# Kernel optimization log

Hardware: AMD Instinct MI355X
Metric: run time of the kernel (lower is better)

## Reference

```python
import jax, jax.numpy as jnp
import numpy as np

NUM_STEPS = 100
ALPHA = 0.9      # learn_alpha=False default in snn.Synaptic
THRESHOLD = 1.0
SLOPE = 25.0     # fast_sigmoid default slope

@jax.custom_vjp
def spike_fn(x):
    # Heaviside forward with fast-sigmoid surrogate gradient
    return (x > 0).astype(x.dtype)

def _spike_fwd(x):
    return (x > 0).astype(x.dtype), x

def _spike_bwd(x, g):
    return (g / (SLOPE * jnp.abs(x) + 1.0) ** 2,)

spike_fn.defvjp(_spike_fwd, _spike_bwd)


def setup_inputs() -> dict:
    key = jax.random.key(0)
    k0, k1, k2 = jax.random.split(key, 3)
    B, NI, NH, NO = 4096, 256, 2048, 128
    x = jax.random.normal(k0, (B, NI), dtype=jnp.float32)
    # Linear init scale ~ 1/sqrt(fan_in)
    W1 = jax.random.normal(k1, (NH, NI), dtype=jnp.float32) / np.sqrt(NI)
    b1 = jnp.zeros((NH,), dtype=jnp.float32)
    W2 = jax.random.normal(k2, (NO, NH), dtype=jnp.float32) / np.sqrt(NH)
    b2 = jnp.zeros((NO,), dtype=jnp.float32)
    beta = jnp.asarray(0.85, dtype=jnp.float32)  # learnable scalar
    return {"x": x, "W1": W1, "b1": b1, "W2": W2, "b2": b2, "beta": beta}


def reference(x, W1, b1, W2, b2, beta):
    # cur1 = fc1(x) is identical every step -> hoist (same math)
    cur1 = x @ W1.T + b1                      # [B, NH]
    beta_c = jnp.clip(beta, 0.0, 1.0)
    B, NH = cur1.shape
    z = jnp.zeros((B, NH), dtype=cur1.dtype)

    def step(carry, _):
        syn, mem, _spk = carry
        # reset-by-subtraction from detached pre-update membrane
        reset = jax.lax.stop_gradient((mem > THRESHOLD).astype(mem.dtype))
        syn = ALPHA * syn + cur1
        mem = beta_c * mem + syn - reset * THRESHOLD
        spk = spike_fn(mem - THRESHOLD)
        return (syn, mem, spk), None

    (syn, mem, spk), _ = jax.lax.scan(step, (z, z, z), None, length=NUM_STEPS)
    cur2 = spk @ W2.T + b2                    # [B, NO]
    return cur2
```

## Files before the change

kernel.cpp:

```cpp
#include <hip/hip_runtime.h>
#include <stdint.h>


typedef __attribute__((ext_vector_type(8))) short short8;
typedef __attribute__((ext_vector_type(4))) float floatx4;

#define NSTEPS 100

static __device__ __forceinline__ uint32_t f2bf2(float lo, float hi) {
  union { float f; uint32_t u; } a, b; a.f = lo; b.f = hi;
  uint32_t x = (a.u + 0x7FFFu + ((a.u >> 16) & 1u)) >> 16;
  uint32_t y = (b.u + 0x7FFFu + ((b.u >> 16) & 1u)) & 0xFFFF0000u;
  return x | y;
}

__global__ __launch_bounds__(256, 4) void snn_k1(
    const float* __restrict__ X, const float* __restrict__ W1,
    const float* __restrict__ b1, const float* __restrict__ betap,
    uint16_t* __restrict__ spk)
{
  __shared__ __align__(16) float As[32 * 68];
  __shared__ __align__(16) float Bs[32 * 68];
  const int tid = threadIdx.x;
  const int bm  = blockIdx.y * 64;
  const int bn  = blockIdx.x * 64;
  const int ty  = tid >> 4;
  const int tx  = tid & 15;
  const int sc  = tid & 7;
  const int sr  = tid >> 3;

  float acc[4][4] = {};

  float4 xa[2], wa[2];
  #pragma unroll
  for (int h = 0; h < 2; ++h) {
    const int r = sr + h * 32;
    xa[h] = *(const float4*)(X  + (size_t)(bm + r) * 256 + sc * 4);
    wa[h] = *(const float4*)(W1 + (size_t)(bn + r) * 256 + sc * 4);
  }

  #pragma unroll 1
  for (int k0 = 0; k0 < 256; k0 += 32) {
    #pragma unroll
    for (int h = 0; h < 2; ++h) {
      const int r = sr + h * 32;
      As[(sc * 4 + 0) * 68 + r] = xa[h].x;
      As[(sc * 4 + 1) * 68 + r] = xa[h].y;
      As[(sc * 4 + 2) * 68 + r] = xa[h].z;
      As[(sc * 4 + 3) * 68 + r] = xa[h].w;
      Bs[(sc * 4 + 0) * 68 + r] = wa[h].x;
      Bs[(sc * 4 + 1) * 68 + r] = wa[h].y;
      Bs[(sc * 4 + 2) * 68 + r] = wa[h].z;
      Bs[(sc * 4 + 3) * 68 + r] = wa[h].w;
    }
    __syncthreads();

    if (k0 < 224) {
      const int kn = k0 + 32;
      #pragma unroll
      for (int h = 0; h < 2; ++h) {
        const int r = sr + h * 32;
        xa[h] = *(const float4*)(X  + (size_t)(bm + r) * 256 + kn + sc * 4);
        wa[h] = *(const float4*)(W1 + (size_t)(bn + r) * 256 + kn + sc * 4);
      }
    }

    #pragma unroll
    for (int kk = 0; kk < 32; ++kk) {
      const float4 a4 = *(const float4*)(As + kk * 68 + ty * 4);
      const float4 b4 = *(const float4*)(Bs + kk * 68 + tx * 4);
      const float av[4] = {a4.x, a4.y, a4.z, a4.w};
      const float bv[4] = {b4.x, b4.y, b4.z, b4.w};
      #pragma unroll
      for (int i = 0; i < 4; ++i)
        #pragma unroll
        for (int j = 0; j < 4; ++j)
          acc[i][j] += av[i] * bv[j];
    }
    __syncthreads();
  }

  float beta = betap[0];
  beta = fminf(fmaxf(beta, 0.0f), 1.0f);
  float bias[4];
  #pragma unroll
  for (int j = 0; j < 4; ++j) bias[j] = b1[bn + tx * 4 + j];

  float cc[16];
  #pragma unroll
  for (int i = 0; i < 4; ++i)
    #pragma unroll
    for (int j = 0; j < 4; ++j)
      cc[i * 4 + j] = acc[i][j] + bias[j];

  #pragma unroll
  for (int h = 0; h < 2; ++h) {
    float syn[8], mem[8];
    #pragma unroll
    for (int e = 0; e < 8; ++e) { syn[e] = 0.0f; mem[e] = 0.0f; }

    #pragma unroll 1
    for (int t = 0; t < NSTEPS; ++t) {
      #pragma unroll
      for (int e = 0; e < 8; ++e) {
        const float rst = (mem[e] > 1.0f) ? 1.0f : 0.0f;
        syn[e] = __fadd_rn(__fmul_rn(0.9f, syn[e]), cc[h * 8 + e]);
        mem[e] = __fsub_rn(__fadd_rn(__fmul_rn(beta, mem[e]), syn[e]), rst);
      }
    }

    #pragma unroll
    for (int i = 0; i < 2; ++i) {
      ushort4 o;
      o.x = (mem[i * 4 + 0] > 1.0f) ? (uint16_t)0x3F80u : (uint16_t)0u;
      o.y = (mem[i * 4 + 1] > 1.0f) ? (uint16_t)0x3F80u : (uint16_t)0u;
      o.z = (mem[i * 4 + 2] > 1.0f) ? (uint16_t)0x3F80u : (uint16_t)0u;
      o.w = (mem[i * 4 + 3] > 1.0f) ? (uint16_t)0x3F80u : (uint16_t)0u;
      *(ushort4*)(spk + (size_t)(bm + ty * 4 + h * 2 + i) * 2048 + bn + tx * 4) = o;
    }
  }
}

#define PS 72

__global__ __launch_bounds__(256) void snn_k2(
    const uint16_t* __restrict__ spk, const float* __restrict__ W2,
    float* __restrict__ part)
{
  __shared__ short As[128 * PS];
  __shared__ short Bs[128 * PS];
  const int tid  = threadIdx.x;
  const int lane = tid & 63;
  const int w    = tid >> 6;
  const int wm   = (w >> 1) * 64;
  const int wn   = (w & 1) * 64;
  const int bm   = blockIdx.x * 128;
  const int kc   = blockIdx.y;

  floatx4 acc[4][4] = {};

  #pragma unroll 1
  for (int kk = 0; kk < 4; ++kk) {
    const int k0 = kc * 256 + kk * 64;
    #pragma unroll
    for (int p = 0; p < 4; ++p) {
      const int u = p * 256 + tid;
      const int r = u >> 3, c = u & 7;
      const int4 va = *(const int4*)(spk + (size_t)(bm + r) * 2048 + k0 + c * 8);
      *(int4*)(As + r * PS + c * 8) = va;
    }
    #pragma unroll
    for (int p = 0; p < 4; ++p) {
      const int u = p * 256 + tid;
      const int n = u >> 3, c = u & 7;
      const float* wp = W2 + (size_t)n * 2048 + k0 + c * 8;
      const float4 w0 = *(const float4*)(wp);
      const float4 w1 = *(const float4*)(wp + 4);
      int4 pk;
      pk.x = (int)f2bf2(w0.x, w0.y);
      pk.y = (int)f2bf2(w0.z, w0.w);
      pk.z = (int)f2bf2(w1.x, w1.y);
      pk.w = (int)f2bf2(w1.z, w1.w);
      *(int4*)(Bs + n * PS + c * 8) = pk;
    }
    __syncthreads();

    #pragma unroll
    for (int ks = 0; ks < 2; ++ks) {
      const int kb = ks * 4 + (lane >> 4);
      const int fe = lane & 15;
      short8 a8[4], b8[4];
      #pragma unroll
      for (int tm = 0; tm < 4; ++tm)
        a8[tm] = *(const short8*)(As + (wm + tm * 16 + fe) * PS + kb * 8);
      #pragma unroll
      for (int tn = 0; tn < 4; ++tn)
        b8[tn] = *(const short8*)(Bs + (wn + tn * 16 + fe) * PS + kb * 8);
      #pragma unroll
      for (int tm = 0; tm < 4; ++tm)
        #pragma unroll
        for (int tn = 0; tn < 4; ++tn)
          acc[tm][tn] = __builtin_amdgcn_mfma_f32_16x16x32_bf16(
              a8[tm], b8[tn], acc[tm][tn], 0, 0, 0);
    }
    __syncthreads();
  }

  const int fe = lane & 15;
  const int fr = (lane >> 4) * 4;
  #pragma unroll
  for (int tm = 0; tm < 4; ++tm)
    #pragma unroll
    for (int tn = 0; tn < 4; ++tn)
      #pragma unroll
      for (int r = 0; r < 4; ++r) {
        const int row = bm + wm + tm * 16 + fr + r;
        const int col = wn + tn * 16 + fe;
        part[((size_t)kc * 4096 + row) * 128 + col] = acc[tm][tn][r];
      }
}

__global__ __launch_bounds__(256) void snn_k3(
    const float* __restrict__ part, const float* __restrict__ b2,
    float* __restrict__ out)
{
  const int idx = blockIdx.x * 256 + threadIdx.x;
  const int m = idx >> 5;
  const int c = (idx & 31) << 2;
  float s0 = 0.f, s1 = 0.f, s2 = 0.f, s3 = 0.f;
  #pragma unroll
  for (int kc = 0; kc < 8; ++kc) {
    const float4 p = *(const float4*)(part + ((size_t)kc * 4096 + m) * 128 + c);
    s0 += p.x; s1 += p.y; s2 += p.z; s3 += p.w;
  }
  float4 o;
  o.x = s0 + b2[c + 0];
  o.y = s1 + b2[c + 1];
  o.z = s2 + b2[c + 2];
  o.w = s3 + b2[c + 3];
  *(float4*)(out + (size_t)m * 128 + c) = o;
}

extern "C" void kernel_launch(void* const* d_in, const int* in_sizes, int n_in,
                              void* d_out, int out_size, void* d_ws, size_t ws_size,
                              hipStream_t stream) {
  const float* X    = (const float*)d_in[0];
  const float* W1   = (const float*)d_in[1];
  const float* b1   = (const float*)d_in[2];
  const float* W2   = (const float*)d_in[3];
  const float* b2   = (const float*)d_in[4];
  const float* beta = (const float*)d_in[5];
  float* out = (float*)d_out;

  uint16_t* spk = (uint16_t*)d_ws;
  float* part = (float*)((char*)d_ws + (size_t)4096 * 2048 * 2);

  snn_k1<<<dim3(32, 64), 256, 0, stream>>>(X, W1, b1, beta, spk);
  snn_k2<<<dim3(32, 8), 256, 0, stream>>>(spk, W2, part);
  snn_k3<<<512, 256, 0, stream>>>(part, b2, out);
}
```

Baseline: 212.1 us.

## Double k1 K-tile and restructure k2 into LDS-free register-fed MFMA with more blocks

The first kernel now stages a 64-wide K slice per iteration instead of 32, which halves the number of barrier and prefetch rounds at the cost of twice the shared memory. The second kernel drops its shared-memory staging entirely. Each wave loads its spike and W2 fragments straight from global memory into MFMA operands over smaller 32x128 output tiles, and the grid grows from 32 to 128 blocks along M. This trades operand reuse through LDS for more parallelism and no barriers, so W2 is re-read and converted to bf16 by more blocks.

```diff
diff --git a/kernel.cpp b/kernel.cpp
--- a/kernel.cpp
+++ b/kernel.cpp
@@ -19,8 +19,8 @@
     const float* __restrict__ b1, const float* __restrict__ betap,
     uint16_t* __restrict__ spk)
 {
-  __shared__ __align__(16) float As[32 * 68];
-  __shared__ __align__(16) float Bs[32 * 68];
+  __shared__ __align__(16) float As[64 * 68];
+  __shared__ __align__(16) float Bs[64 * 68];
   const int tid = threadIdx.x;
   const int bm  = blockIdx.y * 64;
   const int bn  = blockIdx.x * 64;
@@ -31,42 +31,52 @@
 
   float acc[4][4] = {};
 
-  float4 xa[2], wa[2];
+  float4 xa[2][2], wa[2][2];
   #pragma unroll
   for (int h = 0; h < 2; ++h) {
     const int r = sr + h * 32;
-    xa[h] = *(const float4*)(X  + (size_t)(bm + r) * 256 + sc * 4);
-    wa[h] = *(const float4*)(W1 + (size_t)(bn + r) * 256 + sc * 4);
+    #pragma unroll
+    for (int kh = 0; kh < 2; ++kh) {
+      xa[h][kh] = *(const float4*)(X  + (size_t)(bm + r) * 256 + kh * 32 + sc * 4);
+      wa[h][kh] = *(const float4*)(W1 + (size_t)(bn + r) * 256 + kh * 32 + sc * 4);
+    }
   }
 
   #pragma unroll 1
-  for (int k0 = 0; k0 < 256; k0 += 32) {
+  for (int k0 = 0; k0 < 256; k0 += 64) {
     #pragma unroll
     for (int h = 0; h < 2; ++h) {
       const int r = sr + h * 32;
-      As[(sc * 4 + 0) * 68 + r] = xa[h].x;
-      As[(sc * 4 + 1) * 68 + r] = xa[h].y;
-      As[(sc * 4 + 2) * 68 + r] = xa[h].z;
-      As[(sc * 4 + 3) * 68 + r] = xa[h].w;
-      Bs[(sc * 4 + 0) * 68 + r] = wa[h].x;
-      Bs[(sc * 4 + 1) * 68 + r] = wa[h].y;
-      Bs[(sc * 4 + 2) * 68 + r] = wa[h].z;
-      Bs[(sc * 4 + 3) * 68 + r] = wa[h].w;
+      #pragma unroll
+      for (int kh = 0; kh < 2; ++kh) {
+        const int kb = kh * 32 + sc * 4;
+        As[(kb + 0) * 68 + r] = xa[h][kh].x;
+        As[(kb + 1) * 68 + r] = xa[h][kh].y;
+        As[(kb + 2) * 68 + r] = xa[h][kh].z;
+        As[(kb + 3) * 68 + r] = xa[h][kh].w;
+        Bs[(kb + 0) * 68 + r] = wa[h][kh].x;
+        Bs[(kb + 1) * 68 + r] = wa[h][kh].y;
+        Bs[(kb + 2) * 68 + r] = wa[h][kh].z;
+        Bs[(kb + 3) * 68 + r] = wa[h][kh].w;
+      }
     }
     __syncthreads();
 
-    if (k0 < 224) {
-      const int kn = k0 + 32;
+    if (k0 < 192) {
+      const int kn = k0 + 64;
       #pragma unroll
       for (int h = 0; h < 2; ++h) {
         const int r = sr + h * 32;
-        xa[h] = *(const float4*)(X  + (size_t)(bm + r) * 256 + kn + sc * 4);
-        wa[h] = *(const float4*)(W1 + (size_t)(bn + r) * 256 + kn + sc * 4);
-      }
-    }
-
-    #pragma unroll
-    for (int kk = 0; kk < 32; ++kk) {
+        #pragma unroll
+        for (int kh = 0; kh < 2; ++kh) {
+          xa[h][kh] = *(const float4*)(X  + (size_t)(bm + r) * 256 + kn + kh * 32 + sc * 4);
+          wa[h][kh] = *(const float4*)(W1 + (size_t)(bn + r) * 256 + kn + kh * 32 + sc * 4);
+        }
+      }
+    }
+
+    #pragma unroll
+    for (int kk = 0; kk < 64; ++kk) {
       const float4 a4 = *(const float4*)(As + kk * 68 + ty * 4);
       const float4 b4 = *(const float4*)(Bs + kk * 68 + tx * 4);
       const float av[4] = {a4.x, a4.y, a4.z, a4.w};
@@ -121,80 +131,59 @@
   }
 }
 
-#define PS 72
-
 __global__ __launch_bounds__(256) void snn_k2(
     const uint16_t* __restrict__ spk, const float* __restrict__ W2,
     float* __restrict__ part)
 {
-  __shared__ short As[128 * PS];
-  __shared__ short Bs[128 * PS];
   const int tid  = threadIdx.x;
   const int lane = tid & 63;
   const int w    = tid >> 6;
-  const int wm   = (w >> 1) * 64;
-  const int wn   = (w & 1) * 64;
-  const int bm   = blockIdx.x * 128;
+  const int wn   = w * 32;
+  const int bm   = blockIdx.x * 32;
   const int kc   = blockIdx.y;
-
-  floatx4 acc[4][4] = {};
-
-  #pragma unroll 1
-  for (int kk = 0; kk < 4; ++kk) {
-    const int k0 = kc * 256 + kk * 64;
-    #pragma unroll
-    for (int p = 0; p < 4; ++p) {
-      const int u = p * 256 + tid;
-      const int r = u >> 3, c = u & 7;
-      const int4 va = *(const int4*)(spk + (size_t)(bm + r) * 2048 + k0 + c * 8);
-      *(int4*)(As + r * PS + c * 8) = va;
-    }
-    #pragma unroll
-    for (int p = 0; p < 4; ++p) {
-      const int u = p * 256 + tid;
-      const int n = u >> 3, c = u & 7;
-      const float* wp = W2 + (size_t)n * 2048 + k0 + c * 8;
+  const int fe   = lane & 15;
+  const int kq   = lane >> 4;
+
+  floatx4 acc[2][2] = {};
+
+  const uint16_t* a0 = spk + (size_t)(bm + fe) * 2048 + kc * 256 + kq * 8;
+  const uint16_t* a1 = a0 + (size_t)16 * 2048;
+  const float* b0 = W2 + (size_t)(wn + fe) * 2048 + kc * 256 + kq * 8;
+  const float* b1p = b0 + (size_t)16 * 2048;
+
+  #pragma unroll
+  for (int kb = 0; kb < 8; ++kb) {
+    const int ko = kb * 32;
+    short8 a8[2], b8[2];
+    a8[0] = *(const short8*)(a0 + ko);
+    a8[1] = *(const short8*)(a1 + ko);
+    #pragma unroll
+    for (int tn = 0; tn < 2; ++tn) {
+      const float* wp = (tn == 0) ? (b0 + ko) : (b1p + ko);
       const float4 w0 = *(const float4*)(wp);
       const float4 w1 = *(const float4*)(wp + 4);
-      int4 pk;
-      pk.x = (int)f2bf2(w0.x, w0.y);
-      pk.y = (int)f2bf2(w0.z, w0.w);
-      pk.z = (int)f2bf2(w1.x, w1.y);
-      pk.w = (int)f2bf2(w1.z, w1.w);
-      *(int4*)(Bs + n * PS + c * 8) = pk;
-    }
-    __syncthreads();
-
-    #pragma unroll
-    for (int ks = 0; ks < 2; ++ks) {
-      const int kb = ks * 4 + (lane >> 4);
-      const int fe = lane & 15;
-      short8 a8[4], b8[4];
-      #pragma unroll
-      for (int tm = 0; tm < 4; ++tm)
-        a8[tm] = *(const short8*)(As + (wm + tm * 16 + fe) * PS + kb * 8);
-      #pragma unroll
-      for (int tn = 0; tn < 4; ++tn)
-        b8[tn] = *(const short8*)(Bs + (wn + tn * 16 + fe) * PS + kb * 8);
-      #pragma unroll
-      for (int tm = 0; tm < 4; ++tm)
-        #pragma unroll
-        for (int tn = 0; tn < 4; ++tn)
-          acc[tm][tn] = __builtin_amdgcn_mfma_f32_16x16x32_bf16(
-              a8[tm], b8[tn], acc[tm][tn], 0, 0, 0);
-    }
-    __syncthreads();
-  }
-
-  const int fe = lane & 15;
-  const int fr = (lane >> 4) * 4;
-  #pragma unroll
-  for (int tm = 0; tm < 4; ++tm)
-    #pragma unroll
-    for (int tn = 0; tn < 4; ++tn)
+      union { int4 i4; short8 s8; } pk;
+      pk.i4.x = (int)f2bf2(w0.x, w0.y);
+      pk.i4.y = (int)f2bf2(w0.z, w0.w);
+      pk.i4.z = (int)f2bf2(w1.x, w1.y);
+      pk.i4.w = (int)f2bf2(w1.z, w1.w);
+      b8[tn] = pk.s8;
+    }
+    #pragma unroll
+    for (int tm = 0; tm < 2; ++tm)
+      #pragma unroll
+      for (int tn = 0; tn < 2; ++tn)
+        acc[tm][tn] = __builtin_amdgcn_mfma_f32_16x16x32_bf16(
+            a8[tm], b8[tn], acc[tm][tn], 0, 0, 0);
+  }
+
+  #pragma unroll
+  for (int tm = 0; tm < 2; ++tm)
+    #pragma unroll
+    for (int tn = 0; tn < 2; ++tn)
       #pragma unroll
       for (int r = 0; r < 4; ++r) {
-        const int row = bm + wm + tm * 16 + fr + r;
+        const int row = bm + tm * 16 + kq * 4 + r;
         const int col = wn + tn * 16 + fe;
         part[((size_t)kc * 4096 + row) * 128 + col] = acc[tm][tn][r];
       }
@@ -236,6 +225,6 @@
   float* part = (float*)((char*)d_ws + (size_t)4096 * 2048 * 2);
 
   snn_k1<<<dim3(32, 64), 256, 0, stream>>>(X, W1, b1, beta, spk);
-  snn_k2<<<dim3(32, 8), 256, 0, stream>>>(spk, W2, part);
+  snn_k2<<<dim3(128, 8), 256, 0, stream>>>(spk, W2, part);
   snn_k3<<<512, 256, 0, stream>>>(part, b2, out);
 }
```

After: 265.5 us. +25.1%, slower.

## Split GEMM1 and recurrence into separate kernels with larger GEMM tiles

Applied to the files above, without the earlier changes.

The fused GEMM+LIF kernel is split into a 128x128-tile fp32 GEMM that writes cur1 to workspace and a separate elementwise kernel that runs the 100-step recurrence and writes bf16 spikes. The hidden dimension is processed in two halves of 1024 so the cur1 buffer fits in the reused partial-sum workspace. Larger tiles raise arithmetic intensity of GEMM1 and the recurrence kernel gets full occupancy. The cost is an extra round trip of cur1 through global memory and four launches instead of one.

```diff
diff --git a/kernel.cpp b/kernel.cpp
--- a/kernel.cpp
+++ b/kernel.cpp
@@ -14,111 +14,135 @@
   return x | y;
 }
 
-__global__ __launch_bounds__(256, 4) void snn_k1(
-    const float* __restrict__ X, const float* __restrict__ W1,
-    const float* __restrict__ b1, const float* __restrict__ betap,
-    uint16_t* __restrict__ spk)
-{
-  __shared__ __align__(16) float As[32 * 68];
-  __shared__ __align__(16) float Bs[32 * 68];
+__global__ __launch_bounds__(256) void snn_gemm1(
+    const float* __restrict__ X, const float* __restrict__ W1h,
+    const float* __restrict__ b1h, float* __restrict__ cur1h)
+{
+  __shared__ __align__(16) float As[32 * 132];
+  __shared__ __align__(16) float Bs[32 * 132];
   const int tid = threadIdx.x;
-  const int bm  = blockIdx.y * 64;
-  const int bn  = blockIdx.x * 64;
+  const int bn  = blockIdx.x * 128;
+  const int bm  = blockIdx.y * 128;
   const int ty  = tid >> 4;
   const int tx  = tid & 15;
+  const int sr  = tid >> 3;
   const int sc  = tid & 7;
-  const int sr  = tid >> 3;
-
-  float acc[4][4] = {};
-
-  float4 xa[2], wa[2];
-  #pragma unroll
-  for (int h = 0; h < 2; ++h) {
-    const int r = sr + h * 32;
-    xa[h] = *(const float4*)(X  + (size_t)(bm + r) * 256 + sc * 4);
-    wa[h] = *(const float4*)(W1 + (size_t)(bn + r) * 256 + sc * 4);
+
+  float acc[8][8] = {};
+
+  float4 xa[4], wa[4];
+  #pragma unroll
+  for (int h = 0; h < 4; ++h) {
+    const int r = h * 32 + sr;
+    xa[h] = *(const float4*)(X   + (size_t)(bm + r) * 256 + sc * 4);
+    wa[h] = *(const float4*)(W1h + (size_t)(bn + r) * 256 + sc * 4);
   }
 
   #pragma unroll 1
   for (int k0 = 0; k0 < 256; k0 += 32) {
     #pragma unroll
-    for (int h = 0; h < 2; ++h) {
-      const int r = sr + h * 32;
-      As[(sc * 4 + 0) * 68 + r] = xa[h].x;
-      As[(sc * 4 + 1) * 68 + r] = xa[h].y;
-      As[(sc * 4 + 2) * 68 + r] = xa[h].z;
-      As[(sc * 4 + 3) * 68 + r] = xa[h].w;
-      Bs[(sc * 4 + 0) * 68 + r] = wa[h].x;
-      Bs[(sc * 4 + 1) * 68 + r] = wa[h].y;
-      Bs[(sc * 4 + 2) * 68 + r] = wa[h].z;
-      Bs[(sc * 4 + 3) * 68 + r] = wa[h].w;
+    for (int h = 0; h < 4; ++h) {
+      const int r = h * 32 + sr;
+      As[(sc * 4 + 0) * 132 + r] = xa[h].x;
+      As[(sc * 4 + 1) * 132 + r] = xa[h].y;
+      As[(sc * 4 + 2) * 132 + r] = xa[h].z;
+      As[(sc * 4 + 3) * 132 + r] = xa[h].w;
+      Bs[(sc * 4 + 0) * 132 + r] = wa[h].x;
+      Bs[(sc * 4 + 1) * 132 + r] = wa[h].y;
+      Bs[(sc * 4 + 2) * 132 + r] = wa[h].z;
+      Bs[(sc * 4 + 3) * 132 + r] = wa[h].w;
     }
     __syncthreads();
 
     if (k0 < 224) {
       const int kn = k0 + 32;
       #pragma unroll
-      for (int h = 0; h < 2; ++h) {
-        const int r = sr + h * 32;
-        xa[h] = *(const float4*)(X  + (size_t)(bm + r) * 256 + kn + sc * 4);
-        wa[h] = *(const float4*)(W1 + (size_t)(bn + r) * 256 + kn + sc * 4);
+      for (int h = 0; h < 4; ++h) {
+        const int r = h * 32 + sr;
+        xa[h] = *(const float4*)(X   + (size_t)(bm + r) * 256 + kn + sc * 4);
+        wa[h] = *(const float4*)(W1h + (size_t)(bn + r) * 256 + kn + sc * 4);
       }
     }
 
     #pragma unroll
     for (int kk = 0; kk < 32; ++kk) {
-      const float4 a4 = *(const float4*)(As + kk * 68 + ty * 4);
-      const float4 b4 = *(const float4*)(Bs + kk * 68 + tx * 4);
-      const float av[4] = {a4.x, a4.y, a4.z, a4.w};
-      const float bv[4] = {b4.x, b4.y, b4.z, b4.w};
-      #pragma unroll
-      for (int i = 0; i < 4; ++i)
+      const float4 a0 = *(const float4*)(As + kk * 132 + ty * 8);
+      const float4 a1 = *(const float4*)(As + kk * 132 + ty * 8 + 4);
+      const float4 b0 = *(const float4*)(Bs + kk * 132 + tx * 8);
+      const float4 b1 = *(const float4*)(Bs + kk * 132 + tx * 8 + 4);
+      const float av[8] = {a0.x, a0.y, a0.z, a0.w, a1.x, a1.y, a1.z, a1.w};
+      const float bv[8] = {b0.x, b0.y, b0.z, b0.w, b1.x, b1.y, b1.z, b1.w};
+      #pragma unroll
+      for (int i = 0; i < 8; ++i)
         #pragma unroll
-        for (int j = 0; j < 4; ++j)
+        for (int j = 0; j < 8; ++j)
           acc[i][j] += av[i] * bv[j];
     }
     __syncthreads();
   }
+
+  float bias[8];
+  #pragma unroll
+  for (int j = 0; j < 8; ++j) bias[j] = b1h[bn + tx * 8 + j];
+
+  #pragma unroll
+  for (int i = 0; i < 8; ++i) {
+    const int row = bm + ty * 8 + i;
+    float4 o0, o1;
+    o0.x = acc[i][0] + bias[0];
+    o0.y = acc[i][1] + bias[1];
+    o0.z = acc[i][2] + bias[2];
+    o0.w = acc[i][3] + bias[3];
+    o1.x = acc[i][4] + bias[4];
+    o1.y = acc[i][5] + bias[5];
+    o1.z = acc[i][6] + bias[6];
+    o1.w = acc[i][7] + bias[7];
+    *(float4*)(cur1h + (size_t)row * 1024 + bn + tx * 8)     = o0;
+    *(float4*)(cur1h + (size_t)row * 1024 + bn + tx * 8 + 4) = o1;
+  }
+}
+
+__global__ __launch_bounds__(256) void snn_rec(
+    const float* __restrict__ cur1h, const float* __restrict__ betap,
+    uint16_t* __restrict__ spk, int nh0)
+{
+  const int idx = blockIdx.x * 256 + threadIdx.x;
+  const int row = idx >> 7;
+  const int col = (idx & 127) * 8;
+
+  const float4 c0 = *(const float4*)(cur1h + (size_t)row * 1024 + col);
+  const float4 c1 = *(const float4*)(cur1h + (size_t)row * 1024 + col + 4);
+  const float cc[8] = {c0.x, c0.y, c0.z, c0.w, c1.x, c1.y, c1.z, c1.w};
 
   float beta = betap[0];
   beta = fminf(fmaxf(beta, 0.0f), 1.0f);
-  float bias[4];
-  #pragma unroll
-  for (int j = 0; j < 4; ++j) bias[j] = b1[bn + tx * 4 + j];
-
-  float cc[16];
-  #pragma unroll
-  for (int i = 0; i < 4; ++i)
-    #pragma unroll
-    for (int j = 0; j < 4; ++j)
-      cc[i * 4 + j] = acc[i][j] + bias[j];
-
-  #pragma unroll
-  for (int h = 0; h < 2; ++h) {
-    float syn[8], mem[8];
-    #pragma unroll
-    for (int e = 0; e < 8; ++e) { syn[e] = 0.0f; mem[e] = 0.0f; }
-
-    #pragma unroll 1
-    for (int t = 0; t < NSTEPS; ++t) {
-      #pragma unroll
-      for (int e = 0; e < 8; ++e) {
-        const float rst = (mem[e] > 1.0f) ? 1.0f : 0.0f;
-        syn[e] = __fadd_rn(__fmul_rn(0.9f, syn[e]), cc[h * 8 + e]);
-        mem[e] = __fsub_rn(__fadd_rn(__fmul_rn(beta, mem[e]), syn[e]), rst);
-      }
-    }
-
-    #pragma unroll
-    for (int i = 0; i < 2; ++i) {
-      ushort4 o;
-      o.x = (mem[i * 4 + 0] > 1.0f) ? (uint16_t)0x3F80u : (uint16_t)0u;
-      o.y = (mem[i * 4 + 1] > 1.0f) ? (uint16_t)0x3F80u : (uint16_t)0u;
-      o.z = (mem[i * 4 + 2] > 1.0f) ? (uint16_t)0x3F80u : (uint16_t)0u;
-      o.w = (mem[i * 4 + 3] > 1.0f) ? (uint16_t)0x3F80u : (uint16_t)0u;
-      *(ushort4*)(spk + (size_t)(bm + ty * 4 + h * 2 + i) * 2048 + bn + tx * 4) = o;
-    }
-  }
+
+  float syn[8], mem[8];
+  #pragma unroll
+  for (int e = 0; e < 8; ++e) { syn[e] = 0.0f; mem[e] = 0.0f; }
+
+  #pragma unroll 1
+  for (int t = 0; t < NSTEPS; ++t) {
+    #pragma unroll
+    for (int e = 0; e < 8; ++e) {
+      const float rst = (mem[e] > 1.0f) ? 1.0f : 0.0f;
+      syn[e] = __fadd_rn(__fmul_rn(0.9f, syn[e]), cc[e]);
+      mem[e] = __fsub_rn(__fadd_rn(__fmul_rn(beta, mem[e]), syn[e]), rst);
+    }
+  }
+
+  ushort4 o0, o1;
+  o0.x = (mem[0] > 1.0f) ? (uint16_t)0x3F80u : (uint16_t)0u;
+  o0.y = (mem[1] > 1.0f) ? (uint16_t)0x3F80u : (uint16_t)0u;
+  o0.z = (mem[2] > 1.0f) ? (uint16_t)0x3F80u : (uint16_t)0u;
+  o0.w = (mem[3] > 1.0f) ? (uint16_t)0x3F80u : (uint16_t)0u;
+  o1.x = (mem[4] > 1.0f) ? (uint16_t)0x3F80u : (uint16_t)0u;
+  o1.y = (mem[5] > 1.0f) ? (uint16_t)0x3F80u : (uint16_t)0u;
+  o1.z = (mem[6] > 1.0f) ? (uint16_t)0x3F80u : (uint16_t)0u;
+  o1.w = (mem[7] > 1.0f) ? (uint16_t)0x3F80u : (uint16_t)0u;
+  uint16_t* sp = spk + (size_t)row * 2048 + nh0 + col;
+  *(ushort4*)(sp)     = o0;
+  *(ushort4*)(sp + 4) = o1;
 }
 
 #define PS 72
@@ -233,9 +257,15 @@
   float* out = (float*)d_out;
 
   uint16_t* spk = (uint16_t*)d_ws;
-  float* part = (float*)((char*)d_ws + (size_t)4096 * 2048 * 2);
-
-  snn_k1<<<dim3(32, 64), 256, 0, stream>>>(X, W1, b1, beta, spk);
+  float* part   = (float*)((char*)d_ws + (size_t)4096 * 2048 * 2);
+  float* cur1h = part;
+
+  snn_gemm1<<<dim3(8, 32), 256, 0, stream>>>(X, W1, b1, cur1h);
+  snn_rec<<<2048, 256, 0, stream>>>(cur1h, beta, spk, 0);
+  snn_gemm1<<<dim3(8, 32), 256, 0, stream>>>(
+      X, W1 + (size_t)1024 * 256, b1 + 1024, cur1h);
+  snn_rec<<<2048, 256, 0, stream>>>(cur1h, beta, spk, 1024);
+
   snn_k2<<<dim3(32, 8), 256, 0, stream>>>(spk, W2, part);
   snn_k3<<<512, 256, 0, stream>>>(part, b2, out);
 }
```

Result: slower. 236.2 us (+11.3%).
